# Performance work log

Measured on AMD Instinct MI355X. Metric: run time of the kernel, lower is better.

Reference implementation:

```python
import jax, jax.numpy as jnp
import numpy as np

N_HEADS = 16
MAX_CACHE_LEN = 8192
LN_EPS = 1e-5


def _layernorm(x, g, b):
    mu = jnp.mean(x, axis=-1, keepdims=True)
    var = jnp.var(x, axis=-1, keepdims=True)
    return (x - mu) * jax.lax.rsqrt(var + LN_EPS) * g + b


def setup_inputs() -> dict:
    key = jax.random.key(0)
    ks = jax.random.split(key, 8)
    b, t, d, latdim, past = 2, 2048, 2048, 512, 2048
    s = 0.02
    return {
        "x": jax.random.normal(ks[0], (b, t, d), jnp.float32),
        "latent_prev": jax.random.normal(ks[1], (b, past, latdim), jnp.float32),
        "Wq": jax.random.normal(ks[2], (d, d), jnp.float32) * s,
        "Wdown": jax.random.normal(ks[3], (d, latdim), jnp.float32) * s,
        "Wk_up": jax.random.normal(ks[4], (latdim, d), jnp.float32) * s,
        "Wv_up": jax.random.normal(ks[5], (latdim, d), jnp.float32) * s,
        "ln_g": jnp.ones((latdim,), jnp.float32),
        "ln_b": jnp.zeros((latdim,), jnp.float32),
        "Wo": jax.random.normal(ks[6], (d, d), jnp.float32) * s,
    }


def reference(x, latent_prev, Wq, Wdown, Wk_up, Wv_up, ln_g, ln_b, Wo):
    b, t, d = x.shape
    H = N_HEADS
    hd = d // H
    # q projection -> [b, t, H, hd]
    q = (x @ Wq).reshape(b, t, H, hd)
    # latent down-projection + LayerNorm, concat with cache, trim to max_cache_len
    latent_new = _layernorm(x @ Wdown, ln_g, ln_b)
    latent = jnp.concatenate([latent_prev, latent_new], axis=1)
    latent = latent[:, -MAX_CACHE_LEN:]
    S = latent.shape[1]
    past_len = min(latent_prev.shape[1], S - t)
    # up-project K/V from latent -> [b, S, H, hd]
    k = (latent @ Wk_up).reshape(b, S, H, hd)
    v = (latent @ Wv_up).reshape(b, S, H, hd)
    # offset-causal SDPA: query i attends keys j <= past_len + i
    scores = jnp.einsum("bthd,bshd->bhts", q, k) / jnp.sqrt(jnp.asarray(hd, x.dtype))
    i = jnp.arange(t)[:, None]
    j = jnp.arange(S)[None, :]
    mask = j <= (past_len + i)  # [t, S]
    scores = jnp.where(mask[None, None], scores, jnp.asarray(-1e30, scores.dtype))
    attn = jax.nn.softmax(scores, axis=-1)
    out = jnp.einsum("bhts,bshd->bthd", attn, v).reshape(b, t, d)
    return out @ Wo
```

## Files before the change

### kernel.cpp

```cpp
#include <hip/hip_runtime.h>
#include <hip/hip_bf16.h>

using bf16_t = __bf16;
typedef __bf16 bf16x8 __attribute__((ext_vector_type(8)));
typedef __bf16 bf16x4 __attribute__((ext_vector_type(4)));
typedef __bf16 bf16x2 __attribute__((ext_vector_type(2)));
typedef float  f32x4  __attribute__((ext_vector_type(4)));
typedef float  f32x16 __attribute__((ext_vector_type(16)));
typedef unsigned u32x4 __attribute__((ext_vector_type(4)));

#define MFMA16(a,b,c) __builtin_amdgcn_mfma_f32_16x16x32_bf16((a),(b),(c),0,0,0)
#define MFMA32(a,b,c) __builtin_amdgcn_mfma_f32_32x32x16_bf16((a),(b),(c),0,0,0)

__device__ __forceinline__ void load_lds16(const void* g, void* l) {
  __builtin_amdgcn_global_load_lds(
      (const __attribute__((address_space(1))) unsigned int*)g,
      (__attribute__((address_space(3))) unsigned int*)l, 16, 0, 0);
}

__device__ __forceinline__ unsigned pack_bf16(float a, float b) {
  union { bf16x2 v; unsigned u; } c;
  c.v[0] = (bf16_t)a; c.v[1] = (bf16_t)b;
  return c.u;
}

__device__ __forceinline__ float fast_exp2(float x) {
#if __has_builtin(__builtin_amdgcn_exp2f)
  return __builtin_amdgcn_exp2f(x);
#else
  return exp2f(x);
#endif
}

__global__ __launch_bounds__(256) void cvt_f2b(const float* __restrict__ in,
                                               bf16_t* __restrict__ out)
{
  const size_t i = ((size_t)blockIdx.x * 256 + threadIdx.x) * 4;
  f32x4 d = *(const f32x4*)(in + i);
  bf16x4 o;
#pragma unroll
  for (int j = 0; j < 4; ++j) o[j] = (bf16_t)d[j];
  *(bf16x4*)(out + i) = o;
}

__global__ __launch_bounds__(256) void cvt_transpose(const float* __restrict__ in,
                                                     bf16_t* __restrict__ out,
                                                     int R, int C)
{
  __shared__ __align__(16) bf16_t t[64 * 80];
  const int r0 = blockIdx.y * 64, c0 = blockIdx.x * 64;
  const int rr = threadIdx.x >> 4;
  const int c4 = (threadIdx.x & 15) * 4;
#pragma unroll
  for (int i = 0; i < 4; ++i) {
    const int r = rr + i * 16;
    f32x4 d = *(const f32x4*)(in + (size_t)(r0 + r) * C + c0 + c4);
#pragma unroll
    for (int j = 0; j < 4; ++j) t[(c4 + j) * 80 + r] = (bf16_t)d[j];
  }
  __syncthreads();
  const int a  = threadIdx.x >> 3;
  const int bc = (threadIdx.x & 7) * 8;
#pragma unroll
  for (int half = 0; half < 2; ++half) {
    const int cc = a + half * 32;
    bf16x8 d = *(const bf16x8*)&t[cc * 80 + bc];
    *(bf16x8*)(out + (size_t)(c0 + cc) * R + r0 + bc) = d;
  }
}

template <typename OutT>
__global__ __launch_bounds__(256) void gemm128(const bf16_t* __restrict__ A,
                                               const bf16_t* __restrict__ BT,
                                               OutT* __restrict__ C,
                                               int M, int N, int K, float scale,
                                               long long zB, long long zC)
{
  __shared__ __align__(16) bf16_t As[128 * 32];
  __shared__ __align__(16) bf16_t Bs[128 * 32];
  const int tid = threadIdx.x;
  BT += (size_t)blockIdx.z * zB;
  C  += (size_t)blockIdx.z * zC;
  const int m0 = blockIdx.y * 128, n0 = blockIdx.x * 128;
  const int lane = tid & 63, w = tid >> 6;
  const int quad = lane >> 4, l15 = lane & 15;
  const int wm = (w >> 1) * 64, wn = (w & 1) * 64;
  const int s_row = tid >> 2;
  const int g_off = ((tid & 3) ^ (s_row & 3)) * 8;
  const int quadp = (quad ^ (l15 & 3)) * 8;
  const bf16_t* Ap0 = A  + (size_t)(m0 + s_row) * K + g_off;
  const bf16_t* Ap1 = A  + (size_t)(m0 + 64 + s_row) * K + g_off;
  const bf16_t* Bp0 = BT + (size_t)(n0 + s_row) * K + g_off;
  const bf16_t* Bp1 = BT + (size_t)(n0 + 64 + s_row) * K + g_off;

  f32x4 acc[4][4] = {};

  for (int k0 = 0; k0 < K; k0 += 32) {
    __syncthreads();
    load_lds16(Ap0 + k0, As + tid * 8);
    load_lds16(Ap1 + k0, As + tid * 8 + 2048);
    load_lds16(Bp0 + k0, Bs + tid * 8);
    load_lds16(Bp1 + k0, Bs + tid * 8 + 2048);
    __syncthreads();
    bf16x8 af[4], bfr[4];
#pragma unroll
    for (int fi = 0; fi < 4; ++fi)
      af[fi] = *(const bf16x8*)&As[(wm + fi * 16 + l15) * 32 + quadp];
#pragma unroll
    for (int fj = 0; fj < 4; ++fj)
      bfr[fj] = *(const bf16x8*)&Bs[(wn + fj * 16 + l15) * 32 + quadp];
#pragma unroll
    for (int fi = 0; fi < 4; ++fi)
#pragma unroll
      for (int fj = 0; fj < 4; ++fj)
        acc[fi][fj] = MFMA16(af[fi], bfr[fj], acc[fi][fj]);
  }

#pragma unroll
  for (int fi = 0; fi < 4; ++fi)
#pragma unroll
    for (int fj = 0; fj < 4; ++fj)
#pragma unroll
      for (int r = 0; r < 4; ++r) {
        const int row = m0 + wm + fi * 16 + quad * 4 + r;
        const int col = n0 + wn + fj * 16 + l15;
        C[(size_t)row * N + col] = (OutT)(acc[fi][fj][r] * scale);
      }
}

__global__ __launch_bounds__(256) void copy_prev_f(const float* __restrict__ prev,
                                                   bf16_t* __restrict__ latent)
{
  const size_t v    = (size_t)blockIdx.x * 256 + threadIdx.x;
  const size_t flat = v * 4;
  const size_t per  = (size_t)2048 * 512;
  const size_t b    = flat / per, rem = flat % per;
  f32x4 d = *(const f32x4*)(prev + flat);
  bf16x4 o;
#pragma unroll
  for (int j = 0; j < 4; ++j) o[j] = (bf16_t)d[j];
  *(bf16x4*)(latent + b * ((size_t)4096 * 512) + rem) = o;
}

__global__ __launch_bounds__(256) void ln_kernel(const bf16_t* __restrict__ in,
                                                 const float* __restrict__ g_,
                                                 const float* __restrict__ b_,
                                                 bf16_t* __restrict__ latent)
{
  const int row = blockIdx.x;
  const int tid = threadIdx.x;
  const float x0 = (float)in[(size_t)row * 512 + tid];
  const float x1 = (float)in[(size_t)row * 512 + 256 + tid];
  float s  = x0 + x1;
  float sq = x0 * x0 + x1 * x1;
#pragma unroll
  for (int off = 1; off < 64; off <<= 1) {
    s  += __shfl_xor(s, off);
    sq += __shfl_xor(sq, off);
  }
  __shared__ float red[8];
  const int w = tid >> 6;
  if ((tid & 63) == 0) { red[w] = s; red[4 + w] = sq; }
  __syncthreads();
  s  = red[0] + red[1] + red[2] + red[3];
  sq = red[4] + red[5] + red[6] + red[7];
  const float mu   = s * (1.0f / 512.0f);
  const float var  = sq * (1.0f / 512.0f) - mu * mu;
  const float rstd = rsqrtf(var + 1e-5f);
  const int b = row >> 11, tt = row & 2047;
  bf16_t* outp = latent + ((size_t)b * 4096 + 2048 + tt) * 512;
  outp[tid]       = (bf16_t)((x0 - mu) * rstd * g_[tid]       + b_[tid]);
  outp[tid + 256] = (bf16_t)((x1 - mu) * rstd * g_[tid + 256] + b_[tid + 256]);
}

__global__ __launch_bounds__(256) void attn3(const bf16_t* __restrict__ q,
                                             const bf16_t* __restrict__ k,
                                             const bf16_t* __restrict__ vT,
                                             bf16_t* __restrict__ out)
{
  __shared__ __align__(16) bf16_t smem[32768];

  const int tid = threadIdx.x;
  const int lane = tid & 63, w = tid >> 6;
  const int l31 = lane & 31, h5 = lane >> 5;
  int qt = blockIdx.x;
  if (blockIdx.z) qt = 15 - qt;
  const int h = blockIdx.y, b = blockIdx.z;
  const int q0 = qt * 128;
  const int qg = q0 + l31 * 4 + w;

  bf16x8 qf[8];
  const bf16_t* qb = q + ((size_t)(b * 2048 + qg)) * 2048 + h * 128 + h5 * 8;
#pragma unroll
  for (int fc = 0; fc < 8; ++fc) qf[fc] = *(const bf16x8*)(qb + fc * 16);

  const bf16_t* kbase = k + ((size_t)b * 4096) * 2048 + h * 128;
  const bf16_t* vbase = vT + ((size_t)(b * 16 + h)) * 128 * 4096;

  int ks_key[4], ks_go[4], vs_feat[4], vs_go[4];
#pragma unroll
  for (int p = 0; p < 4; ++p) {
    const int slot = tid + 256 * p;
    const int key = slot >> 4, ph = slot & 15;
    ks_key[p] = key;
    ks_go[p]  = (((ph & 8) | ((ph & 7) ^ (key & 7)))) * 8;
    const int ft = slot >> 3, p2 = slot & 7;
    vs_feat[p] = ft;
    vs_go[p]   = (p2 ^ (ft & 7)) * 8;
  }
  int kfo[8], vfo[4];
#pragma unroll
  for (int fc = 0; fc < 8; ++fc) {
    const int L = fc * 2 + h5;
    kfo[fc] = l31 * 128 + ((L & 8) | ((L & 7) ^ (l31 & 7))) * 8;
  }
#pragma unroll
  for (int kc = 0; kc < 4; ++kc) {
    const int L = kc * 2 + h5;
    vfo[kc] = l31 * 64 + (L ^ (l31 & 7)) * 8;
  }

  f32x16 o[4] = {};
  float m = -1e30f, l = 0.f;
  const int send = 2048 + q0 + 128;

#pragma unroll
  for (int p = 0; p < 4; ++p) {
    load_lds16(kbase + (size_t)ks_key[p] * 2048 + ks_go[p],
               smem + (tid + 256 * p) * 8);
    load_lds16(vbase + (size_t)vs_feat[p] * 4096 + vs_go[p],
               smem + 16384 + (tid + 256 * p) * 8);
  }
  __syncthreads();

  int cur = 0;
  for (int s0 = 0; s0 < send; s0 += 64) {
    const int s1 = s0 + 64;
    if (s1 < send) {
      const int nxt = (cur ^ 1) * 8192;
#pragma unroll
      for (int p = 0; p < 4; ++p) {
        load_lds16(kbase + (size_t)(s1 + ks_key[p]) * 2048 + ks_go[p],
                   smem + nxt + (tid + 256 * p) * 8);
        load_lds16(vbase + (size_t)vs_feat[p] * 4096 + s1 + vs_go[p],
                   smem + 16384 + nxt + (tid + 256 * p) * 8);
      }
    }
    const bf16_t* Kc = smem + cur * 8192;
    const bf16_t* Vc = smem + 16384 + cur * 8192;

    f32x16 st[2] = {};
    __builtin_amdgcn_s_setprio(1);
#pragma unroll
    for (int fc = 0; fc < 8; ++fc) {
      bf16x8 k0 = *(const bf16x8*)&Kc[kfo[fc]];
      bf16x8 k1 = *(const bf16x8*)&Kc[4096 + kfo[fc]];
      st[0] = MFMA32(k0, qf[fc], st[0]);
      st[1] = MFMA32(k1, qf[fc], st[1]);
    }
    __builtin_amdgcn_s_setprio(0);

    if (s0 + 63 > 2048 + q0) {
#pragma unroll
      for (int t = 0; t < 2; ++t)
#pragma unroll
        for (int i = 0; i < 16; ++i) {
          const int key = s0 + 32 * t + (i & 3) + 8 * (i >> 2) + 4 * h5;
          if (key > 2048 + qg) st[t][i] = -1e30f;
        }
    }

    float gm[8];
#pragma unroll
    for (int t = 0; t < 2; ++t)
#pragma unroll
      for (int g = 0; g < 4; ++g)
        gm[t * 4 + g] = fmaxf(fmaxf(st[t][4 * g + 0], st[t][4 * g + 1]),
                              fmaxf(st[t][4 * g + 2], st[t][4 * g + 3]));
    float mt = fmaxf(fmaxf(fmaxf(gm[0], gm[1]), fmaxf(gm[2], gm[3])),
                     fmaxf(fmaxf(gm[4], gm[5]), fmaxf(gm[6], gm[7])));
    mt = fmaxf(mt, __shfl_xor(mt, 32));

    if (__any(mt > m + 8.f)) {
      const float mnew = fmaxf(m, mt);
      const float alpha = fast_exp2(m - mnew);
#pragma unroll
      for (int ft = 0; ft < 4; ++ft)
#pragma unroll
        for (int i = 0; i < 16; ++i) o[ft][i] *= alpha;
      l *= alpha;
      m = mnew;
    }

    float rs = 0.f;
    unsigned up[2][4][2];
#pragma unroll
    for (int t = 0; t < 2; ++t)
#pragma unroll
      for (int g = 0; g < 4; ++g) {
        const float p0 = fast_exp2(st[t][4 * g + 0] - m);
        const float p1 = fast_exp2(st[t][4 * g + 1] - m);
        const float p2 = fast_exp2(st[t][4 * g + 2] - m);
        const float p3 = fast_exp2(st[t][4 * g + 3] - m);
        rs += (p0 + p1) + (p2 + p3);
        up[t][g][0] = pack_bf16(p0, p1);
        up[t][g][1] = pack_bf16(p2, p3);
      }
    rs += __shfl_xor(rs, 32);
    l += rs;

#pragma unroll
    for (int kc = 0; kc < 4; ++kc) {
      const int t = kc >> 1, gp = (kc & 1) * 2;
      const unsigned a0 = up[t][gp][0],     a1 = up[t][gp][1];
      const unsigned b0 = up[t][gp + 1][0], b1 = up[t][gp + 1][1];
      const unsigned xa0 = __shfl_xor(a0, 32), xa1 = __shfl_xor(a1, 32);
      const unsigned xb0 = __shfl_xor(b0, 32), xb1 = __shfl_xor(b1, 32);
      u32x4 uw;
      uw[0] = h5 ? xb0 : a0;
      uw[1] = h5 ? xb1 : a1;
      uw[2] = h5 ? b0 : xa0;
      uw[3] = h5 ? b1 : xa1;
      union { u32x4 u; bf16x8 v; } pc; pc.u = uw;
      const bf16x8 pf = pc.v;
      __builtin_amdgcn_s_setprio(1);
#pragma unroll
      for (int ft = 0; ft < 4; ++ft) {
        bf16x8 vf = *(const bf16x8*)&Vc[ft * 2048 + vfo[kc]];
        o[ft] = MFMA32(vf, pf, o[ft]);
      }
      __builtin_amdgcn_s_setprio(0);
    }

    __syncthreads();
    cur ^= 1;
  }

  const float inv = 1.0f / l;
  const int rowp_w = w * 32 + l31;
#pragma unroll
  for (int ft = 0; ft < 4; ++ft)
#pragma unroll
    for (int g = 0; g < 4; ++g) {
      bf16x4 pk;
#pragma unroll
      for (int r = 0; r < 4; ++r) pk[r] = (bf16_t)(o[ft][4 * g + r] * inv);
      *(bf16x4*)&smem[rowp_w * 136 + ft * 32 + g * 8 + h5 * 4] = pk;
    }
  __syncthreads();
#pragma unroll
  for (int p = 0; p < 8; ++p) {
    const int c = tid + 256 * p;
    const int rowp = c >> 4, chk = c & 15;
    const int ql = (rowp & 31) * 4 + (rowp >> 5);
    bf16x8 d = *(const bf16x8*)&smem[rowp * 136 + chk * 8];
    *(bf16x8*)(out + ((size_t)(b * 2048 + q0 + ql)) * 2048 + h * 128 + chk * 8) = d;
  }
}

extern "C" void kernel_launch(void* const* d_in, const int* in_sizes, int n_in,
                              void* d_out, int out_size, void* d_ws, size_t ws_size,
                              hipStream_t stream)
{
  (void)in_sizes; (void)n_in; (void)out_size; (void)ws_size;
  const float* x        = (const float*)d_in[0];
  const float* lat_prev = (const float*)d_in[1];
  const float* Wq       = (const float*)d_in[2];
  const float* Wdown    = (const float*)d_in[3];
  const float* Wk_up    = (const float*)d_in[4];
  const float* Wv_up    = (const float*)d_in[5];
  const float* ln_g     = (const float*)d_in[6];
  const float* ln_b     = (const float*)d_in[7];
  const float* Wo       = (const float*)d_in[8];
  float* out = (float*)d_out;

  char* p = (char*)d_ws;
  auto alloc = [&](size_t elems) { bf16_t* r = (bf16_t*)p; p += elems * 2; return r; };
  bf16_t* xb     = alloc((size_t)4096 * 2048);
  bf16_t* WqT    = alloc((size_t)2048 * 2048);
  bf16_t* WdT    = alloc((size_t)512 * 2048);
  bf16_t* qbuf   = alloc((size_t)4096 * 2048);
  bf16_t* latpre = alloc((size_t)4096 * 512);
  bf16_t* latent = alloc((size_t)2 * 4096 * 512);
  bf16_t* kbuf   = alloc((size_t)8192 * 2048);
  bf16_t* vTb    = alloc((size_t)2 * 2048 * 4096);
  bf16_t* aout   = alloc((size_t)4096 * 2048);
  bf16_t* WoT  = xb;
  bf16_t* WkT  = latpre;
  bf16_t* WvT  = latpre + (size_t)2048 * 512;

  const dim3 B(256);
  const float qscale = 0.12751744561825988f;

  cvt_f2b<<<dim3(8192), B, 0, stream>>>(x, xb);
  cvt_transpose<<<dim3(32, 32), B, 0, stream>>>(Wq,    WqT, 2048, 2048);
  cvt_transpose<<<dim3(8,  32), B, 0, stream>>>(Wdown, WdT, 2048, 512);
  gemm128<bf16_t><<<dim3(16, 32), B, 0, stream>>>(xb, WqT, qbuf, 4096, 2048, 2048, qscale, 0, 0);
  gemm128<bf16_t><<<dim3(4,  32), B, 0, stream>>>(xb, WdT, latpre, 4096, 512, 2048, 1.0f, 0, 0);
  copy_prev_f<<<dim3(2048), B, 0, stream>>>(lat_prev, latent);
  ln_kernel<<<dim3(4096), B, 0, stream>>>(latpre, ln_g, ln_b, latent);
  cvt_transpose<<<dim3(32, 32), B, 0, stream>>>(Wo,    WoT, 2048, 2048);
  cvt_transpose<<<dim3(32, 8),  B, 0, stream>>>(Wk_up, WkT, 512, 2048);
  cvt_transpose<<<dim3(32, 8),  B, 0, stream>>>(Wv_up, WvT, 512, 2048);
  gemm128<bf16_t><<<dim3(16, 64), B, 0, stream>>>(latent, WkT, kbuf, 8192, 2048, 512, 1.0f, 0, 0);
  gemm128<bf16_t><<<dim3(32, 16, 2), B, 0, stream>>>(WvT, latent, vTb, 2048, 4096, 512, 1.0f,
                                                     (long long)4096 * 512,
                                                     (long long)2048 * 4096);
  attn3<<<dim3(16, 16, 2), B, 0, stream>>>(qbuf, kbuf, vTb, aout);
  gemm128<float><<<dim3(16, 32), B, 0, stream>>>(aout, WoT, out, 4096, 2048, 2048, 1.0f, 0, 0);
}
```

Before: 581.0 us.

## Split attention KV range across two blocks and stream V from global

Attention is split so each (query tile, head, batch) is processed by two blocks covering halves of the key range. The partial outputs and per-row max/sum go to workspace, and a new combine kernel merges them. V is no longer staged in LDS but loaded directly from global into registers, with one-chunk-ahead prefetch. Shrinking LDS lets launch_bounds request 3 blocks per CU. This adds a combine pass, extra workspace traffic and less reuse of V, in exchange for better load balance and occupancy.

```diff
diff --git a/kernel.cpp b/kernel.cpp
--- a/kernel.cpp
+++ b/kernel.cpp
@@ -173,21 +173,42 @@
   outp[tid + 256] = (bf16_t)((x1 - mu) * rstd * g_[tid + 256] + b_[tid + 256]);
 }
 
-__global__ __launch_bounds__(256) void attn3(const bf16_t* __restrict__ q,
-                                             const bf16_t* __restrict__ k,
-                                             const bf16_t* __restrict__ vT,
-                                             bf16_t* __restrict__ out)
-{
-  __shared__ __align__(16) bf16_t smem[32768];
+template <bool SPLIT>
+__global__ __launch_bounds__(256, 3) void attn4(const bf16_t* q,
+                                                const bf16_t* k,
+                                                const bf16_t* vT,
+                                                bf16_t* out0, bf16_t* out1,
+                                                float2* ml)
+{
+  __shared__ __align__(16) bf16_t smem[17408];
 
   const int tid = threadIdx.x;
   const int lane = tid & 63, w = tid >> 6;
   const int l31 = lane & 31, h5 = lane >> 5;
-  int qt = blockIdx.x;
-  if (blockIdx.z) qt = 15 - qt;
-  const int h = blockIdx.y, b = blockIdx.z;
+
+  int qt, h, b, half;
+  if (SPLIT) {
+    const int g = blockIdx.x & 7, j = blockIdx.x >> 3;
+    h = g + 8 * (j >> 6);
+    const int r = j & 63;
+    qt = r & 15;
+    b  = (r >> 4) & 1;
+    half = r >> 5;
+  } else {
+    qt = blockIdx.x & 15;
+    h  = (blockIdx.x >> 4) & 15;
+    b  = blockIdx.x >> 8;
+    if (b) qt = 15 - qt;
+    half = 0;
+  }
   const int q0 = qt * 128;
   const int qg = q0 + l31 * 4 + w;
+  const int qlim = 2048 + q0;
+
+  const int ntot = 34 + 2 * qt;
+  const int nt0  = SPLIT ? (ntot >> 1) : ntot;
+  const int tbeg = (SPLIT && half) ? nt0 : 0;
+  const int tend = (SPLIT && !half) ? nt0 : ntot;
 
   bf16x8 qf[8];
   const bf16_t* qb = q + ((size_t)(b * 2048 + qg)) * 2048 + h * 128 + h5 * 8;
@@ -196,58 +217,43 @@
 
   const bf16_t* kbase = k + ((size_t)b * 4096) * 2048 + h * 128;
   const bf16_t* vbase = vT + ((size_t)(b * 16 + h)) * 128 * 4096;
-
-  int ks_key[4], ks_go[4], vs_feat[4], vs_go[4];
+  const bf16_t* vlane = vbase + (size_t)l31 * 4096 + h5 * 8;
+
+  int ks_key[4], ks_go[4];
 #pragma unroll
   for (int p = 0; p < 4; ++p) {
     const int slot = tid + 256 * p;
     const int key = slot >> 4, ph = slot & 15;
     ks_key[p] = key;
     ks_go[p]  = (((ph & 8) | ((ph & 7) ^ (key & 7)))) * 8;
-    const int ft = slot >> 3, p2 = slot & 7;
-    vs_feat[p] = ft;
-    vs_go[p]   = (p2 ^ (ft & 7)) * 8;
-  }
-  int kfo[8], vfo[4];
+  }
+  int kfo[8];
 #pragma unroll
   for (int fc = 0; fc < 8; ++fc) {
     const int L = fc * 2 + h5;
     kfo[fc] = l31 * 128 + ((L & 8) | ((L & 7) ^ (l31 & 7))) * 8;
   }
-#pragma unroll
-  for (int kc = 0; kc < 4; ++kc) {
-    const int L = kc * 2 + h5;
-    vfo[kc] = l31 * 64 + (L ^ (l31 & 7)) * 8;
-  }
 
   f32x16 o[4] = {};
   float m = -1e30f, l = 0.f;
-  const int send = 2048 + q0 + 128;
-
-#pragma unroll
-  for (int p = 0; p < 4; ++p) {
-    load_lds16(kbase + (size_t)ks_key[p] * 2048 + ks_go[p],
+
+#pragma unroll
+  for (int p = 0; p < 4; ++p)
+    load_lds16(kbase + ((size_t)tbeg * 64 + ks_key[p]) * 2048 + ks_go[p],
                smem + (tid + 256 * p) * 8);
-    load_lds16(vbase + (size_t)vs_feat[p] * 4096 + vs_go[p],
-               smem + 16384 + (tid + 256 * p) * 8);
-  }
   __syncthreads();
 
   int cur = 0;
-  for (int s0 = 0; s0 < send; s0 += 64) {
-    const int s1 = s0 + 64;
-    if (s1 < send) {
+  for (int ti = tbeg; ti < tend; ++ti) {
+    const int s0 = ti * 64;
+    if (ti + 1 < tend) {
       const int nxt = (cur ^ 1) * 8192;
 #pragma unroll
-      for (int p = 0; p < 4; ++p) {
-        load_lds16(kbase + (size_t)(s1 + ks_key[p]) * 2048 + ks_go[p],
+      for (int p = 0; p < 4; ++p)
+        load_lds16(kbase + ((size_t)(s0 + 64) + ks_key[p]) * 2048 + ks_go[p],
                    smem + nxt + (tid + 256 * p) * 8);
-        load_lds16(vbase + (size_t)vs_feat[p] * 4096 + s1 + vs_go[p],
-                   smem + 16384 + nxt + (tid + 256 * p) * 8);
-      }
     }
     const bf16_t* Kc = smem + cur * 8192;
-    const bf16_t* Vc = smem + 16384 + cur * 8192;
 
     f32x16 st[2] = {};
     __builtin_amdgcn_s_setprio(1);
@@ -260,7 +266,7 @@
     }
     __builtin_amdgcn_s_setprio(0);
 
-    if (s0 + 63 > 2048 + q0) {
+    if (s0 + 63 > qlim) {
 #pragma unroll
       for (int t = 0; t < 2; ++t)
 #pragma unroll
@@ -291,6 +297,11 @@
       l *= alpha;
       m = mnew;
     }
+
+    bf16x8 vfrag[4][4];
+#pragma unroll
+    for (int ft = 0; ft < 4; ++ft)
+      vfrag[0][ft] = *(const bf16x8*)(vlane + (size_t)ft * 131072 + s0);
 
     float rs = 0.f;
     unsigned up[2][4][2];
@@ -311,6 +322,12 @@
 
 #pragma unroll
     for (int kc = 0; kc < 4; ++kc) {
+      if (kc < 3) {
+#pragma unroll
+        for (int ft = 0; ft < 4; ++ft)
+          vfrag[kc + 1][ft] =
+              *(const bf16x8*)(vlane + (size_t)ft * 131072 + s0 + (kc + 1) * 16);
+      }
       const int t = kc >> 1, gp = (kc & 1) * 2;
       const unsigned a0 = up[t][gp][0],     a1 = up[t][gp][1];
       const unsigned b0 = up[t][gp + 1][0], b1 = up[t][gp + 1][1];
@@ -325,10 +342,8 @@
       const bf16x8 pf = pc.v;
       __builtin_amdgcn_s_setprio(1);
 #pragma unroll
-      for (int ft = 0; ft < 4; ++ft) {
-        bf16x8 vf = *(const bf16x8*)&Vc[ft * 2048 + vfo[kc]];
-        o[ft] = MFMA32(vf, pf, o[ft]);
-      }
+      for (int ft = 0; ft < 4; ++ft)
+        o[ft] = MFMA32(vfrag[kc][ft], pf, o[ft]);
       __builtin_amdgcn_s_setprio(0);
     }
 
@@ -336,6 +351,7 @@
     cur ^= 1;
   }
 
+  bf16_t* const outp = (SPLIT && half) ? out1 : out0;
   const float inv = 1.0f / l;
   const int rowp_w = w * 32 + l31;
 #pragma unroll
@@ -347,6 +363,8 @@
       for (int r = 0; r < 4; ++r) pk[r] = (bf16_t)(o[ft][4 * g + r] * inv);
       *(bf16x4*)&smem[rowp_w * 136 + ft * 32 + g * 8 + h5 * 4] = pk;
     }
+  if (SPLIT && h5 == 0)
+    ml[((size_t)((half * 2 + b) * 16 + h)) * 2048 + qg] = make_float2(m, l);
   __syncthreads();
 #pragma unroll
   for (int p = 0; p < 8; ++p) {
@@ -354,15 +372,40 @@
     const int rowp = c >> 4, chk = c & 15;
     const int ql = (rowp & 31) * 4 + (rowp >> 5);
     bf16x8 d = *(const bf16x8*)&smem[rowp * 136 + chk * 8];
-    *(bf16x8*)(out + ((size_t)(b * 2048 + q0 + ql)) * 2048 + h * 128 + chk * 8) = d;
-  }
+    *(bf16x8*)(outp + ((size_t)(b * 2048 + q0 + ql)) * 2048 + h * 128 + chk * 8) = d;
+  }
+}
+
+__global__ __launch_bounds__(256) void attn_combine(bf16_t* o0,
+                                                    const bf16_t* o1,
+                                                    const float2* ml)
+{
+  const int row = blockIdx.x;
+  const int tid = threadIdx.x;
+  const int b = row >> 11, t = row & 2047;
+  const int h = tid >> 4;
+  const float2 v0 = ml[((size_t)(b * 16 + h)) * 2048 + t];
+  const float2 v1 = ml[((size_t)((2 + b) * 16 + h)) * 2048 + t];
+  const float M  = fmaxf(v0.x, v1.x);
+  const float w0 = v0.y * fast_exp2(v0.x - M);
+  const float w1 = v1.y * fast_exp2(v1.x - M);
+  const float inv = 1.0f / (w0 + w1);
+  const float a0 = w0 * inv, a1 = w1 * inv;
+  const size_t base = (size_t)row * 2048 + tid * 8;
+  bf16x8 x0 = *(const bf16x8*)(o0 + base);
+  bf16x8 x1 = *(const bf16x8*)(o1 + base);
+  bf16x8 r;
+#pragma unroll
+  for (int j = 0; j < 8; ++j)
+    r[j] = (bf16_t)(a0 * (float)x0[j] + a1 * (float)x1[j]);
+  *(bf16x8*)(o0 + base) = r;
 }
 
 extern "C" void kernel_launch(void* const* d_in, const int* in_sizes, int n_in,
                               void* d_out, int out_size, void* d_ws, size_t ws_size,
                               hipStream_t stream)
 {
-  (void)in_sizes; (void)n_in; (void)out_size; (void)ws_size;
+  (void)in_sizes; (void)n_in; (void)out_size;
   const float* x        = (const float*)d_in[0];
   const float* lat_prev = (const float*)d_in[1];
   const float* Wq       = (const float*)d_in[2];
@@ -385,6 +428,9 @@
   bf16_t* kbuf   = alloc((size_t)8192 * 2048);
   bf16_t* vTb    = alloc((size_t)2 * 2048 * 4096);
   bf16_t* aout   = alloc((size_t)4096 * 2048);
+  bf16_t* opart1 = alloc((size_t)4096 * 2048);
+  float2* mlbuf  = (float2*)p; p += (size_t)2 * 2 * 16 * 2048 * sizeof(float2);
+  const size_t needed = (size_t)(p - (char*)d_ws);
   bf16_t* WoT  = xb;
   bf16_t* WkT  = latpre;
   bf16_t* WvT  = latpre + (size_t)2048 * 512;
@@ -406,6 +452,11 @@
   gemm128<bf16_t><<<dim3(32, 16, 2), B, 0, stream>>>(WvT, latent, vTb, 2048, 4096, 512, 1.0f,
                                                      (long long)4096 * 512,
                                                      (long long)2048 * 4096);
-  attn3<<<dim3(16, 16, 2), B, 0, stream>>>(qbuf, kbuf, vTb, aout);
+  if (ws_size == 0 || ws_size >= needed) {
+    attn4<true><<<dim3(1024), B, 0, stream>>>(qbuf, kbuf, vTb, aout, opart1, mlbuf);
+    attn_combine<<<dim3(4096), B, 0, stream>>>(aout, opart1, mlbuf);
+  } else {
+    attn4<false><<<dim3(512), B, 0, stream>>>(qbuf, kbuf, vTb, aout, nullptr, nullptr);
+  }
   gemm128<float><<<dim3(16, 32), B, 0, stream>>>(aout, WoT, out, 4096, 2048, 2048, 1.0f, 0, 0);
 }
```

New measurement: 718.9 us. 23.7% more time.

## Software-pipeline attention so QK of next tile overlaps PV of current tile

Applied to the files above, without the earlier changes.

Restructures the attention inner loop so the QK^T MFMAs for tile i+1 are issued alongside the PV MFMAs for tile i, with K and V staged separately into ping-pong LDS slots. Softmax statistics for the next tile are computed after both matmul groups, which hides exp/max latency behind MFMA work. The launch grid is also flattened to 1D with a remapped block order that groups heads, likely aimed at L2 locality of K/V. This adds register pressure from keeping the packed probabilities live across iterations, and the staging order has subtle slot reuse that must stay correct.

```diff
diff --git a/kernel.cpp b/kernel.cpp
--- a/kernel.cpp
+++ b/kernel.cpp
@@ -173,7 +173,7 @@
   outp[tid + 256] = (bf16_t)((x1 - mu) * rstd * g_[tid + 256] + b_[tid + 256]);
 }
 
-__global__ __launch_bounds__(256) void attn3(const bf16_t* __restrict__ q,
+__global__ __launch_bounds__(256) void attn6(const bf16_t* __restrict__ q,
                                              const bf16_t* __restrict__ k,
                                              const bf16_t* __restrict__ vT,
                                              bf16_t* __restrict__ out)
@@ -183,11 +183,17 @@
   const int tid = threadIdx.x;
   const int lane = tid & 63, w = tid >> 6;
   const int l31 = lane & 31, h5 = lane >> 5;
-  int qt = blockIdx.x;
-  if (blockIdx.z) qt = 15 - qt;
-  const int h = blockIdx.y, b = blockIdx.z;
+
+  const int g = blockIdx.x & 7, j = blockIdx.x >> 3;
+  int qt = j & 15;
+  const int b = (j >> 4) & 1, hsel = j >> 5;
+  const int h = g + 8 * hsel;
+  if (b) qt = 15 - qt;
+
   const int q0 = qt * 128;
   const int qg = q0 + l31 * 4 + w;
+  const int qlim = 2048 + q0;
+  const int nt = 34 + 2 * qt;
 
   bf16x8 qf[8];
   const bf16_t* qb = q + ((size_t)(b * 2048 + qg)) * 2048 + h * 128 + h5 * 8;
@@ -220,36 +226,25 @@
     vfo[kc] = l31 * 64 + (L ^ (l31 & 7)) * 8;
   }
 
+  auto stageK = [&](int t, int slot) {
+#pragma unroll
+    for (int p = 0; p < 4; ++p)
+      load_lds16(kbase + ((size_t)t * 64 + ks_key[p]) * 2048 + ks_go[p],
+                 smem + slot * 8192 + (tid + 256 * p) * 8);
+  };
+  auto stageV = [&](int t, int slot) {
+#pragma unroll
+    for (int p = 0; p < 4; ++p)
+      load_lds16(vbase + (size_t)vs_feat[p] * 4096 + t * 64 + vs_go[p],
+                 smem + 16384 + slot * 8192 + (tid + 256 * p) * 8);
+  };
+
   f32x16 o[4] = {};
-  float m = -1e30f, l = 0.f;
-  const int send = 2048 + q0 + 128;
-
-#pragma unroll
-  for (int p = 0; p < 4; ++p) {
-    load_lds16(kbase + (size_t)ks_key[p] * 2048 + ks_go[p],
-               smem + (tid + 256 * p) * 8);
-    load_lds16(vbase + (size_t)vs_feat[p] * 4096 + vs_go[p],
-               smem + 16384 + (tid + 256 * p) * 8);
-  }
-  __syncthreads();
-
-  int cur = 0;
-  for (int s0 = 0; s0 < send; s0 += 64) {
-    const int s1 = s0 + 64;
-    if (s1 < send) {
-      const int nxt = (cur ^ 1) * 8192;
-#pragma unroll
-      for (int p = 0; p < 4; ++p) {
-        load_lds16(kbase + (size_t)(s1 + ks_key[p]) * 2048 + ks_go[p],
-                   smem + nxt + (tid + 256 * p) * 8);
-        load_lds16(vbase + (size_t)vs_feat[p] * 4096 + s1 + vs_go[p],
-                   smem + 16384 + nxt + (tid + 256 * p) * 8);
-      }
-    }
-    const bf16_t* Kc = smem + cur * 8192;
-    const bf16_t* Vc = smem + 16384 + cur * 8192;
-
-    f32x16 st[2] = {};
+  float m = 0.f, l = 0.f;
+  unsigned up[2][4][2];
+
+  auto qk = [&](int slot, f32x16* st) {
+    const bf16_t* Kc = smem + slot * 8192;
     __builtin_amdgcn_s_setprio(1);
 #pragma unroll
     for (int fc = 0; fc < 8; ++fc) {
@@ -259,56 +254,10 @@
       st[1] = MFMA32(k1, qf[fc], st[1]);
     }
     __builtin_amdgcn_s_setprio(0);
-
-    if (s0 + 63 > 2048 + q0) {
-#pragma unroll
-      for (int t = 0; t < 2; ++t)
-#pragma unroll
-        for (int i = 0; i < 16; ++i) {
-          const int key = s0 + 32 * t + (i & 3) + 8 * (i >> 2) + 4 * h5;
-          if (key > 2048 + qg) st[t][i] = -1e30f;
-        }
-    }
-
-    float gm[8];
-#pragma unroll
-    for (int t = 0; t < 2; ++t)
-#pragma unroll
-      for (int g = 0; g < 4; ++g)
-        gm[t * 4 + g] = fmaxf(fmaxf(st[t][4 * g + 0], st[t][4 * g + 1]),
-                              fmaxf(st[t][4 * g + 2], st[t][4 * g + 3]));
-    float mt = fmaxf(fmaxf(fmaxf(gm[0], gm[1]), fmaxf(gm[2], gm[3])),
-                     fmaxf(fmaxf(gm[4], gm[5]), fmaxf(gm[6], gm[7])));
-    mt = fmaxf(mt, __shfl_xor(mt, 32));
-
-    if (__any(mt > m + 8.f)) {
-      const float mnew = fmaxf(m, mt);
-      const float alpha = fast_exp2(m - mnew);
-#pragma unroll
-      for (int ft = 0; ft < 4; ++ft)
-#pragma unroll
-        for (int i = 0; i < 16; ++i) o[ft][i] *= alpha;
-      l *= alpha;
-      m = mnew;
-    }
-
-    float rs = 0.f;
-    unsigned up[2][4][2];
-#pragma unroll
-    for (int t = 0; t < 2; ++t)
-#pragma unroll
-      for (int g = 0; g < 4; ++g) {
-        const float p0 = fast_exp2(st[t][4 * g + 0] - m);
-        const float p1 = fast_exp2(st[t][4 * g + 1] - m);
-        const float p2 = fast_exp2(st[t][4 * g + 2] - m);
-        const float p3 = fast_exp2(st[t][4 * g + 3] - m);
-        rs += (p0 + p1) + (p2 + p3);
-        up[t][g][0] = pack_bf16(p0, p1);
-        up[t][g][1] = pack_bf16(p2, p3);
-      }
-    rs += __shfl_xor(rs, 32);
-    l += rs;
-
+  };
+
+  auto pv = [&](int slot) {
+    const bf16_t* Vc = smem + 16384 + slot * 8192;
 #pragma unroll
     for (int kc = 0; kc < 4; ++kc) {
       const int t = kc >> 1, gp = (kc & 1) * 2;
@@ -331,21 +280,99 @@
       }
       __builtin_amdgcn_s_setprio(0);
     }
-
+  };
+
+  auto maskst = [&](int s0, f32x16* st) {
+    if (s0 + 63 > qlim) {
+#pragma unroll
+      for (int t = 0; t < 2; ++t)
+#pragma unroll
+        for (int i = 0; i < 16; ++i) {
+          const int key = s0 + 32 * t + (i & 3) + 8 * (i >> 2) + 4 * h5;
+          if (key > 2048 + qg) st[t][i] = -1e30f;
+        }
+    }
+  };
+
+  auto maxst = [&](const f32x16* st) {
+    float gm[8];
+#pragma unroll
+    for (int t = 0; t < 2; ++t)
+#pragma unroll
+      for (int gg = 0; gg < 4; ++gg)
+        gm[t * 4 + gg] = fmaxf(fmaxf(st[t][4 * gg + 0], st[t][4 * gg + 1]),
+                               fmaxf(st[t][4 * gg + 2], st[t][4 * gg + 3]));
+    float mt = fmaxf(fmaxf(fmaxf(gm[0], gm[1]), fmaxf(gm[2], gm[3])),
+                     fmaxf(fmaxf(gm[4], gm[5]), fmaxf(gm[6], gm[7])));
+    return fmaxf(mt, __shfl_xor(mt, 32));
+  };
+
+  auto exppack = [&](const f32x16* st) {
+    float rs = 0.f;
+#pragma unroll
+    for (int t = 0; t < 2; ++t)
+#pragma unroll
+      for (int gg = 0; gg < 4; ++gg) {
+        const float p0 = fast_exp2(st[t][4 * gg + 0] - m);
+        const float p1 = fast_exp2(st[t][4 * gg + 1] - m);
+        const float p2 = fast_exp2(st[t][4 * gg + 2] - m);
+        const float p3 = fast_exp2(st[t][4 * gg + 3] - m);
+        rs += (p0 + p1) + (p2 + p3);
+        up[t][gg][0] = pack_bf16(p0, p1);
+        up[t][gg][1] = pack_bf16(p2, p3);
+      }
+    rs += __shfl_xor(rs, 32);
+    return rs;
+  };
+
+  stageK(0, 0);
+  stageV(0, 0);
+  if (nt > 1) stageK(1, 1);
+  __syncthreads();
+  {
+    f32x16 st[2] = {};
+    qk(0, st);
+    m = maxst(st);
+    l = exppack(st);
+  }
+
+  for (int i = 0; i + 1 < nt; ++i) {
     __syncthreads();
-    cur ^= 1;
-  }
+    if (i + 2 < nt) stageK(i + 2, i & 1);
+    stageV(i + 1, (i + 1) & 1);
+
+    f32x16 st[2] = {};
+    qk((i + 1) & 1, st);
+    pv(i & 1);
+
+    maskst((i + 1) * 64, st);
+    const float mt = maxst(st);
+    if (__any(mt > m + 8.f)) {
+      const float mnew = fmaxf(m, mt);
+      const float alpha = fast_exp2(m - mnew);
+#pragma unroll
+      for (int ft = 0; ft < 4; ++ft)
+#pragma unroll
+        for (int ii = 0; ii < 16; ++ii) o[ft][ii] *= alpha;
+      l *= alpha;
+      m = mnew;
+    }
+    l += exppack(st);
+  }
+
+  __syncthreads();
+  pv((nt - 1) & 1);
 
   const float inv = 1.0f / l;
   const int rowp_w = w * 32 + l31;
 #pragma unroll
   for (int ft = 0; ft < 4; ++ft)
 #pragma unroll
-    for (int g = 0; g < 4; ++g) {
+    for (int gg = 0; gg < 4; ++gg) {
       bf16x4 pk;
 #pragma unroll
-      for (int r = 0; r < 4; ++r) pk[r] = (bf16_t)(o[ft][4 * g + r] * inv);
-      *(bf16x4*)&smem[rowp_w * 136 + ft * 32 + g * 8 + h5 * 4] = pk;
+      for (int r = 0; r < 4; ++r) pk[r] = (bf16_t)(o[ft][4 * gg + r] * inv);
+      *(bf16x4*)&smem[rowp_w * 136 + ft * 32 + gg * 8 + h5 * 4] = pk;
     }
   __syncthreads();
 #pragma unroll
@@ -406,6 +433,6 @@
   gemm128<bf16_t><<<dim3(32, 16, 2), B, 0, stream>>>(WvT, latent, vTb, 2048, 4096, 512, 1.0f,
                                                      (long long)4096 * 512,
                                                      (long long)2048 * 4096);
-  attn3<<<dim3(16, 16, 2), B, 0, stream>>>(qbuf, kbuf, vTb, aout);
+  attn6<<<dim3(512), B, 0, stream>>>(qbuf, kbuf, vTb, aout);
   gemm128<float><<<dim3(16, 32), B, 0, stream>>>(aout, WoT, out, 4096, 2048, 2048, 1.0f, 0, 0);
 }
```

New measurement: 590.4 us. Within noise of the previous version (+1.6%).
